# Kernel tuning notes

Measured on AMD Instinct MI355X. Metric: run time of the kernel, lower is better.

## Reference

```python
import jax, jax.numpy as jnp
import numpy as np

EPS = 1e-10


def setup_inputs() -> dict:
    key = jax.random.key(0)
    k1, k2 = jax.random.split(key)
    B, N = 4096, 10000
    pred = jax.random.uniform(k1, (B, N), dtype=jnp.float32)
    y = jax.random.randint(k2, (B, N), 0, 2, dtype=jnp.int32)
    return {"pred": pred, "y": y, "lamda": 5}


def reference(pred, y, lamda):
    # per-element weighted BCE-style term:
    #   y==0 -> -log(1 - p + eps); y!=0 -> -lamda * log(p + eps)
    neg_term = -jnp.log1p(-(pred - EPS))          # -log(1 - p + eps)
    pos_term = -lamda * jnp.log(pred + EPS)
    elem = jnp.where(y == 0, neg_term, pos_term)  # [B, N]
    # mean over elements per sample, then mean over batch; keep shape (1,) like torch.zeros(1)
    loss = jnp.mean(elem)
    return loss.reshape(1)
```

## Files before the change

### kernel.cpp

```cpp
#include <hip/hip_runtime.h>
#include <hip/hip_bf16.h>

#define EPS 1e-10f
#define BLOCK 256
#define GRID1 2048
#define TILE_VEC (BLOCK * 8)


__global__ __launch_bounds__(BLOCK) void sparse_loss_stage1(
    const float* __restrict__ pred,
    const int* __restrict__ y,
    const int* __restrict__ lamda_p,
    float* __restrict__ partials,
    long long nvec,
    long long total) {
  const float lam = (float)(*lamda_p);
  float acc = 0.0f;

  const float4* __restrict__ pv = reinterpret_cast<const float4*>(pred);
  const int4* __restrict__ yv = reinterpret_cast<const int4*>(y);

  const long long ntiles = (nvec + TILE_VEC - 1) / TILE_VEC;
  const int tid = threadIdx.x;

#define ELEM(P, Y)                                              \
  {                                                             \
    const bool z = ((Y) == 0);                                  \
    const float a = EPS + (z ? (1.0f - (P)) : (P));             \
    const float c = z ? 1.0f : lam;                             \
    acc = fmaf(c, __logf(a), acc);                              \
  }

  for (long long tile = blockIdx.x; tile < ntiles; tile += gridDim.x) {
    const long long base = tile * TILE_VEC;
    const float4* __restrict__ pt = pv + base;
    const int4* __restrict__ yt = yv + base;
    const long long rem = nvec - base;

    if (rem >= TILE_VEC) {
      float4 p[8];
      int4 yy[8];
#pragma unroll
      for (int k = 0; k < 8; ++k) p[k] = pt[tid + BLOCK * k];
#pragma unroll
      for (int k = 0; k < 8; ++k) yy[k] = yt[tid + BLOCK * k];
#pragma unroll
      for (int k = 0; k < 8; ++k) {
        ELEM(p[k].x, yy[k].x)
        ELEM(p[k].y, yy[k].y)
        ELEM(p[k].z, yy[k].z)
        ELEM(p[k].w, yy[k].w)
      }
    } else {
      for (long long j = tid; j < rem; j += BLOCK) {
        const float4 p = pt[j];
        const int4 yy = yt[j];
        ELEM(p.x, yy.x)
        ELEM(p.y, yy.y)
        ELEM(p.z, yy.z)
        ELEM(p.w, yy.w)
      }
    }
  }

  const long long gtid = (long long)blockIdx.x * BLOCK + tid;
  const long long gstride = (long long)gridDim.x * BLOCK;
  for (long long j = nvec * 4 + gtid; j < total; j += gstride) {
    const float p = pred[j];
    ELEM(p, y[j])
  }
#undef ELEM

  for (int off = 32; off > 0; off >>= 1)
    acc += __shfl_down(acc, off, 64);

  __shared__ float ssum[4];
  const int lane = tid & 63;
  const int wave = tid >> 6;
  if (lane == 0) ssum[wave] = acc;
  __syncthreads();

  if (tid == 0)
    partials[blockIdx.x] = ssum[0] + ssum[1] + ssum[2] + ssum[3];
}

__global__ __launch_bounds__(BLOCK) void sparse_loss_stage2(
    const float* __restrict__ partials,
    float* __restrict__ out,
    float inv_total) {
  float acc = 0.0f;
  for (int i = threadIdx.x; i < GRID1; i += BLOCK)
    acc += partials[i];

  for (int off = 32; off > 0; off >>= 1)
    acc += __shfl_down(acc, off, 64);

  __shared__ float ssum[4];
  const int lane = threadIdx.x & 63;
  const int wave = threadIdx.x >> 6;
  if (lane == 0) ssum[wave] = acc;
  __syncthreads();

  if (threadIdx.x == 0)
    out[0] = -(ssum[0] + ssum[1] + ssum[2] + ssum[3]) * inv_total;
}

extern "C" void kernel_launch(void* const* d_in, const int* in_sizes, int n_in,
                              void* d_out, int out_size, void* d_ws, size_t ws_size,
                              hipStream_t stream) {
  const float* pred = (const float*)d_in[0];
  const int* y = (const int*)d_in[1];
  const int* lamda = (const int*)d_in[2];
  float* out = (float*)d_out;
  float* partials = (float*)d_ws;

  const long long total = (long long)in_sizes[0];
  const long long nvec = total / 4;
  const float inv_total = 1.0f / (float)total;

  sparse_loss_stage1<<<GRID1, BLOCK, 0, stream>>>(pred, y, lamda, partials,
                                                  nvec, total);
  sparse_loss_stage2<<<1, BLOCK, 0, stream>>>(partials, out, inv_total);
}
```

Before: 332.9 us.

## Use inline-asm dwordx4 loads with a sweep-strided tiling and masked tail

Replaces the tile loop of 8 float4s per thread with a sweep over the grid, where each block handles 1024 vec4 groups and each thread issues four pred and four label loads through inline global_load_dwordx4. An explicit waitcnt and sched_barrier fix the order of loads and compute. The partial last sweep is handled with clamped indices and multiplicative masks instead of a branchy remainder loop. Each thread keeps fewer bytes in flight per iteration, and the hand-placed waitcnt blocks the compiler from overlapping the next loads with the current compute.

Measured after the change: 328.9 us. Within noise of the previous version (-1.2%).

```diff
diff --git a/kernel.cpp b/kernel.cpp
--- a/kernel.cpp
+++ b/kernel.cpp
@@ -1,11 +1,16 @@
 #include <hip/hip_runtime.h>
-#include <hip/hip_bf16.h>
 
 #define EPS 1e-10f
 #define BLOCK 256
 #define GRID1 2048
-#define TILE_VEC (BLOCK * 8)
+#define BGROUPS 1024
 
+
+typedef float f32x4 __attribute__((ext_vector_type(4)));
+typedef int   i32x4 __attribute__((ext_vector_type(4)));
+
+#define GLOAD(dst, ptr) \
+  asm volatile("global_load_dwordx4 %0, %1, off" : "=v"(dst) : "v"(ptr))
 
 __global__ __launch_bounds__(BLOCK) void sparse_loss_stage1(
     const float* __restrict__ pred,
@@ -17,70 +22,105 @@
   const float lam = (float)(*lamda_p);
   float acc = 0.0f;
 
-  const float4* __restrict__ pv = reinterpret_cast<const float4*>(pred);
-  const int4* __restrict__ yv = reinterpret_cast<const int4*>(y);
+  const f32x4* __restrict__ pv = reinterpret_cast<const f32x4*>(pred);
+  const i32x4* __restrict__ yv = reinterpret_cast<const i32x4*>(y);
 
-  const long long ntiles = (nvec + TILE_VEC - 1) / TILE_VEC;
-  const int tid = threadIdx.x;
+#define ELEM(P, Y)                                   \
+  {                                                  \
+    const bool z = ((Y) == 0);                       \
+    const float a = EPS + (z ? (1.0f - (P)) : (P));  \
+    const float c = z ? 1.0f : lam;                  \
+    acc = fmaf(c, __logf(a), acc);                   \
+  }
+#define ELEM4(A, B) ELEM(A[0], B[0]) ELEM(A[1], B[1]) ELEM(A[2], B[2]) ELEM(A[3], B[3])
 
-#define ELEM(P, Y)                                              \
-  {                                                             \
-    const bool z = ((Y) == 0);                                  \
-    const float a = EPS + (z ? (1.0f - (P)) : (P));             \
-    const float c = z ? 1.0f : lam;                             \
-    acc = fmaf(c, __logf(a), acc);                              \
+#define ELEMM(P, Y, M)                               \
+  {                                                  \
+    const bool z = ((Y) == 0);                       \
+    const float a = EPS + (z ? (1.0f - (P)) : (P));  \
+    const float c = (z ? 1.0f : lam) * (M);          \
+    acc = fmaf(c, __logf(a), acc);                   \
+  }
+#define ELEM4M(A, B, M) \
+  ELEMM(A[0], B[0], M) ELEMM(A[1], B[1], M) ELEMM(A[2], B[2], M) ELEMM(A[3], B[3], M)
+
+  const long long SWEEP = (long long)GRID1 * BGROUPS;
+  const long long nfull = nvec / SWEEP;
+  const long long j0 = (long long)blockIdx.x * BGROUPS + threadIdx.x;
+
+  for (long long s = 0; s < nfull; ++s) {
+    const long long b = s * SWEEP + j0;
+    const f32x4* pp = pv + b;
+    const i32x4* yp = yv + b;
+    f32x4 a0, a1, a2, a3;
+    i32x4 q0, q1, q2, q3;
+    GLOAD(a0, pp);
+    GLOAD(a1, pp + 256);
+    GLOAD(a2, pp + 512);
+    GLOAD(a3, pp + 768);
+    GLOAD(q0, yp);
+    GLOAD(q1, yp + 256);
+    GLOAD(q2, yp + 512);
+    GLOAD(q3, yp + 768);
+    asm volatile("s_waitcnt vmcnt(0)" ::: "memory");
+    __builtin_amdgcn_sched_barrier(0);
+    ELEM4(a0, q0)
+    ELEM4(a1, q1)
+    ELEM4(a2, q2)
+    ELEM4(a3, q3)
   }
 
-  for (long long tile = blockIdx.x; tile < ntiles; tile += gridDim.x) {
-    const long long base = tile * TILE_VEC;
-    const float4* __restrict__ pt = pv + base;
-    const int4* __restrict__ yt = yv + base;
-    const long long rem = nvec - base;
-
-    if (rem >= TILE_VEC) {
-      float4 p[8];
-      int4 yy[8];
-#pragma unroll
-      for (int k = 0; k < 8; ++k) p[k] = pt[tid + BLOCK * k];
-#pragma unroll
-      for (int k = 0; k < 8; ++k) yy[k] = yt[tid + BLOCK * k];
-#pragma unroll
-      for (int k = 0; k < 8; ++k) {
-        ELEM(p[k].x, yy[k].x)
-        ELEM(p[k].y, yy[k].y)
-        ELEM(p[k].z, yy[k].z)
-        ELEM(p[k].w, yy[k].w)
-      }
-    } else {
-      for (long long j = tid; j < rem; j += BLOCK) {
-        const float4 p = pt[j];
-        const int4 yy = yt[j];
-        ELEM(p.x, yy.x)
-        ELEM(p.y, yy.y)
-        ELEM(p.z, yy.z)
-        ELEM(p.w, yy.w)
-      }
-    }
+  const long long rb = nfull * SWEEP;
+  if (rb + (long long)blockIdx.x * BGROUPS < nvec) {
+    const long long b = rb + j0;
+    const long long jA = b, jB = b + 256, jC = b + 512, jD = b + 768;
+    const float mA = (jA < nvec) ? 1.0f : 0.0f;
+    const float mB = (jB < nvec) ? 1.0f : 0.0f;
+    const float mC = (jC < nvec) ? 1.0f : 0.0f;
+    const float mD = (jD < nvec) ? 1.0f : 0.0f;
+    const long long cA = (jA < nvec) ? jA : 0;
+    const long long cB = (jB < nvec) ? jB : 0;
+    const long long cC = (jC < nvec) ? jC : 0;
+    const long long cD = (jD < nvec) ? jD : 0;
+    f32x4 a0, a1, a2, a3;
+    i32x4 q0, q1, q2, q3;
+    GLOAD(a0, pv + cA);
+    GLOAD(a1, pv + cB);
+    GLOAD(a2, pv + cC);
+    GLOAD(a3, pv + cD);
+    GLOAD(q0, yv + cA);
+    GLOAD(q1, yv + cB);
+    GLOAD(q2, yv + cC);
+    GLOAD(q3, yv + cD);
+    asm volatile("s_waitcnt vmcnt(0)" ::: "memory");
+    __builtin_amdgcn_sched_barrier(0);
+    ELEM4M(a0, q0, mA)
+    ELEM4M(a1, q1, mB)
+    ELEM4M(a2, q2, mC)
+    ELEM4M(a3, q3, mD)
   }
 
-  const long long gtid = (long long)blockIdx.x * BLOCK + tid;
+  const long long gtid = (long long)blockIdx.x * BLOCK + threadIdx.x;
   const long long gstride = (long long)gridDim.x * BLOCK;
   for (long long j = nvec * 4 + gtid; j < total; j += gstride) {
     const float p = pred[j];
     ELEM(p, y[j])
   }
 #undef ELEM
+#undef ELEM4
+#undef ELEMM
+#undef ELEM4M
 
   for (int off = 32; off > 0; off >>= 1)
     acc += __shfl_down(acc, off, 64);
 
   __shared__ float ssum[4];
-  const int lane = tid & 63;
-  const int wave = tid >> 6;
+  const int lane = threadIdx.x & 63;
+  const int wave = threadIdx.x >> 6;
   if (lane == 0) ssum[wave] = acc;
   __syncthreads();
 
-  if (tid == 0)
+  if (threadIdx.x == 0)
     partials[blockIdx.x] = ssum[0] + ssum[1] + ssum[2] + ssum[3];
 }
 
```
